# Kernel optimization log

Measured on AMD Instinct MI355X. Metric: run time of the kernel, lower is better.

The kernel has to match this reference:

```python
import jax, jax.numpy as jnp
import numpy as np
import math

B, S, D = 2, 2048, 2048
H = 16
DK = D // H  # 128
DFF = 5440
THETA = 10000.0
EPS = 1e-5


def setup_inputs() -> dict:
    key = jax.random.key(0)
    ks = jax.random.split(key, 9)
    sc = 0.02
    return {
        "x": jax.random.normal(ks[0], (B, S, D), jnp.float32),
        "wq": jax.random.normal(ks[1], (D, D), jnp.float32) * sc,
        "wk": jax.random.normal(ks[2], (D, D), jnp.float32) * sc,
        "wv": jax.random.normal(ks[3], (D, D), jnp.float32) * sc,
        "wo": jax.random.normal(ks[4], (D, D), jnp.float32) * sc,
        "w1": jax.random.normal(ks[5], (DFF, D), jnp.float32) * sc,
        "w2": jax.random.normal(ks[6], (D, DFF), jnp.float32) * sc,
        "w3": jax.random.normal(ks[7], (DFF, D), jnp.float32) * sc,
        "g_attn": jnp.ones((D,), jnp.float32),
        "g_ffn": jnp.ones((D,), jnp.float32),
    }


def _rmsnorm(x, g):
    xf = x.astype(jnp.float32)
    rms = jnp.sqrt(jnp.mean(xf * xf, axis=-1, keepdims=True) + EPS)
    return (xf / rms * g).astype(x.dtype)


def _rope(x):
    # x: (B, H, S, DK)
    pair = jnp.arange(0, DK, 2, dtype=jnp.float32)
    inv_freq = 1.0 / (THETA ** (pair / DK))            # (DK/2,)
    pos = jnp.arange(S, dtype=jnp.float32)
    ang = pos[:, None] * inv_freq[None, :]             # (S, DK/2)
    cos, sin = jnp.cos(ang), jnp.sin(ang)
    xe, xo = x[..., 0::2], x[..., 1::2]
    oe = xe * cos - xo * sin
    oo = xe * sin + xo * cos
    # interleave even/odd back
    out = jnp.stack([oe, oo], axis=-1).reshape(x.shape)
    return out


def reference(x, wq, wk, wv, wo, w1, w2, w3, g_attn, g_ffn):
    # --- attention sublayer ---
    h = _rmsnorm(x, g_attn)
    q = (h @ wq.T).reshape(B, S, H, DK).transpose(0, 2, 1, 3)
    k = (h @ wk.T).reshape(B, S, H, DK).transpose(0, 2, 1, 3)
    v = (h @ wv.T).reshape(B, S, H, DK).transpose(0, 2, 1, 3)
    q = _rope(q)
    k = _rope(k)
    scores = jnp.einsum("bhqd,bhkd->bhqk", q, k) / math.sqrt(DK)
    causal = jnp.tril(jnp.ones((S, S), dtype=bool))
    scores = jnp.where(causal, scores, jnp.finfo(scores.dtype).min)
    attn = jax.nn.softmax(scores, axis=-1)
    o = jnp.einsum("bhqk,bhkd->bhqd", attn, v)
    o = o.transpose(0, 2, 1, 3).reshape(B, S, D)
    x = x + o @ wo.T
    # --- SwiGLU FFN sublayer ---
    h = _rmsnorm(x, g_ffn)
    a = h @ w1.T
    gate = a * jax.nn.sigmoid(a)
    ff = (gate * (h @ w3.T)) @ w2.T
    return x + ff
```

## Files before the change

### kernel.cpp

```cpp
#include <hip/hip_runtime.h>
#include <cstdint>
#include <cstddef>

typedef float  f32x4  __attribute__((ext_vector_type(4)));
typedef __bf16 bf16x8 __attribute__((ext_vector_type(8)));
typedef unsigned short u16x8 __attribute__((ext_vector_type(8)));
typedef unsigned short u16x4 __attribute__((ext_vector_type(4)));

#define DEV static __device__ __forceinline__

DEV unsigned short f2bfu(float f) { __bf16 b = (__bf16)f; return __builtin_bit_cast(unsigned short, b); }
DEV float bfu2f(unsigned short u) { return (float)__builtin_bit_cast(__bf16, u); }
DEV bf16x8 ldb8(const unsigned short* p) { return __builtin_bit_cast(bf16x8, *(const u16x8*)p); }
DEV float fexp(float x) { return __builtin_amdgcn_exp2f(x * 1.44269504f); }

DEV f32x4 mfma16(bf16x8 a, bf16x8 b, f32x4 c) {
  return __builtin_amdgcn_mfma_f32_16x16x32_bf16(a, b, c, 0, 0, 0);
}

DEV void gload16(const void* g, void* l) {
  __builtin_amdgcn_global_load_lds((const unsigned int*)g, (unsigned int*)l, 16, 0, 0);
}

__global__ __launch_bounds__(256) void conv_cat3(
    const float* __restrict__ s0, const float* __restrict__ s1,
    const float* __restrict__ s2, unsigned short* __restrict__ d)
{
  size_t i = (size_t)blockIdx.x * 256 + threadIdx.x;
  size_t e = i * 4;
  const float* s = e < 4194304 ? s0 : (e < 8388608 ? s1 : s2);
  f32x4 v = *(const f32x4*)(s + (e & 4194303));
  u16x4 o = { f2bfu(v.x), f2bfu(v.y), f2bfu(v.z), f2bfu(v.w) };
  *(u16x4*)(d + e) = o;
}

__global__ __launch_bounds__(256) void conv_plain(
    const float* __restrict__ s, unsigned short* __restrict__ d)
{
  size_t e = ((size_t)blockIdx.x * 256 + threadIdx.x) * 4;
  f32x4 v = *(const f32x4*)(s + e);
  u16x4 o = { f2bfu(v.x), f2bfu(v.y), f2bfu(v.z), f2bfu(v.w) };
  *(u16x4*)(d + e) = o;
}

__global__ __launch_bounds__(256) void conv_w13(
    const float* __restrict__ w1, const float* __restrict__ w3,
    unsigned short* __restrict__ d)
{
  size_t i = (size_t)blockIdx.x * 256 + threadIdx.x;
  size_t e = i * 4;
  int n = (int)(e >> 11), kc = (int)(e & 2047);
  int grp = n >> 4;
  const float* s = (grp & 1) ? w3 : w1;
  size_t off = ((size_t)((grp >> 1) * 16 + (n & 15))) * 2048 + kc;
  f32x4 v = *(const f32x4*)(s + off);
  u16x4 o = { f2bfu(v.x), f2bfu(v.y), f2bfu(v.z), f2bfu(v.w) };
  *(u16x4*)(d + e) = o;
}

template<int EPI>
__global__ __launch_bounds__(256) void gemm_f(
    const unsigned short* __restrict__ A, const unsigned short* __restrict__ B,
    void* __restrict__ D0, void* __restrict__ D1, void* __restrict__ D2,
    const float* __restrict__ auxf, const float* __restrict__ cosT,
    const float* __restrict__ sinT, int M, int N, int K)
{
  __shared__ __align__(16) unsigned short As[128 * 64];
  __shared__ __align__(16) unsigned short Bs[128 * 64];
  const int tid = threadIdx.x, lane = tid & 63, w = tid >> 6;
  const int wr = w >> 1, wc = w & 1, l15 = lane & 15, lg = lane >> 4;
  const int m0 = blockIdx.x * 128, n0 = blockIdx.y * 128;

  const int srow  = tid >> 3;
  const int scol8 = (tid & 7) ^ (srow & 7);
  const unsigned short* Asrc = A + (size_t)(m0 + srow) * K + scol8 * 8;
  const unsigned short* Bsrc = B + (size_t)(n0 + srow) * K + scol8 * 8;

  f32x4 zero = {0.f, 0.f, 0.f, 0.f};
  f32x4 acc[4][4];
#pragma unroll
  for (int i = 0; i < 4; i++)
#pragma unroll
    for (int j = 0; j < 4; j++) acc[i][j] = zero;

  for (int k0 = 0; k0 < K; k0 += 64) {
#pragma unroll
    for (int p = 0; p < 4; ++p) {
      gload16(Asrc + (size_t)(p * 32) * K + k0, As + (p * 256 + w * 64) * 8);
      gload16(Bsrc + (size_t)(p * 32) * K + k0, Bs + (p * 256 + w * 64) * 8);
    }
    __syncthreads();
    bf16x8 af[2][4], bfr[2][4];
#pragma unroll
    for (int kk = 0; kk < 2; ++kk) {
#pragma unroll
      for (int i = 0; i < 4; ++i) {
        int rA = wr * 64 + i * 16 + l15;
        af[kk][i]  = ldb8(As + rA * 64 + ((((kk << 2) | lg)) ^ (rA & 7)) * 8);
        int rB = wc * 64 + i * 16 + l15;
        bfr[kk][i] = ldb8(Bs + rB * 64 + ((((kk << 2) | lg)) ^ (rB & 7)) * 8);
      }
    }
#pragma unroll
    for (int kk = 0; kk < 2; ++kk)
#pragma unroll
      for (int mi = 0; mi < 4; mi++)
#pragma unroll
        for (int ni = 0; ni < 4; ni++)
          acc[mi][ni] = mfma16(af[kk][mi], bfr[kk][ni], acc[mi][ni]);
    __syncthreads();
  }

  if constexpr (EPI == 0) {
    unsigned short* qd = (unsigned short*)D0;
    unsigned short* kd = (unsigned short*)D1;
    unsigned short* vd = (unsigned short*)D2;
#pragma unroll
    for (int mi = 0; mi < 4; mi++) {
#pragma unroll
      for (int ni = 0; ni < 4; ni++) {
        int col = n0 + wc * 64 + ni * 16 + l15;
#pragma unroll
        for (int r = 0; r < 4; r++) {
          int row = m0 + wr * 64 + mi * 16 + lg * 4 + r;
          float v = acc[mi][ni][r];
          if (col < 4096) {
            int d = col & 127, pi = d >> 1, sp = row & 2047;
            float c = cosT[sp * 64 + pi], s = sinT[sp * 64 + pi];
            float part = __shfl_xor(v, 1);
            float res = (d & 1) ? (part * s + v * c) : (v * c - part * s);
            unsigned short* dst = (col < 2048) ? qd : kd;
            dst[(size_t)row * 2048 + (col & 2047)] = f2bfu(res);
          } else {
            int vdc = col - 4096;
            vd[((size_t)((row >> 11) * 2048 + vdc)) * 2048 + (row & 2047)] = f2bfu(v);
          }
        }
      }
    }
  } else if constexpr (EPI == 1 || EPI == 3) {
    float* O = (float*)D0;
#pragma unroll
    for (int mi = 0; mi < 4; mi++)
#pragma unroll
      for (int ni = 0; ni < 4; ni++) {
        int col = n0 + wc * 64 + ni * 16 + l15;
#pragma unroll
        for (int r = 0; r < 4; r++) {
          int row = m0 + wr * 64 + mi * 16 + lg * 4 + r;
          size_t ix = (size_t)row * 2048 + col;
          if constexpr (EPI == 1) O[ix] = auxf[ix] + acc[mi][ni][r];
          else                    O[ix] = O[ix] + acc[mi][ni][r];
        }
      }
  } else if constexpr (EPI == 2) {
    unsigned short* G = (unsigned short*)D0;
#pragma unroll
    for (int mi = 0; mi < 4; mi++)
#pragma unroll
      for (int nj = 0; nj < 2; nj++) {
        int outc = (4 * blockIdx.y + 2 * wc + nj) * 16 + l15;
#pragma unroll
        for (int r = 0; r < 4; r++) {
          int row = m0 + wr * 64 + mi * 16 + lg * 4 + r;
          float a = acc[mi][2 * nj][r];
          float c = acc[mi][2 * nj + 1][r];
          float sg = a / (1.0f + fexp(-a));
          G[(size_t)row * 5440 + outc] = f2bfu(sg * c);
        }
      }
  }
}

__global__ __launch_bounds__(256) void rmsnorm_k(
    const float* __restrict__ x, const float* __restrict__ g,
    unsigned short* __restrict__ out)
{
  int row = blockIdx.x, t = threadIdx.x;
  const float* xr = x + (size_t)row * 2048;
  f32x4 v0 = ((const f32x4*)xr)[t];
  f32x4 v1 = ((const f32x4*)xr)[t + 256];
  float ss = v0.x*v0.x + v0.y*v0.y + v0.z*v0.z + v0.w*v0.w
           + v1.x*v1.x + v1.y*v1.y + v1.z*v1.z + v1.w*v1.w;
  __shared__ float red[256];
  red[t] = ss; __syncthreads();
  for (int sh = 128; sh > 0; sh >>= 1) {
    if (t < sh) red[t] += red[t + sh];
    __syncthreads();
  }
  float rinv = rsqrtf(red[0] * (1.0f / 2048.0f) + 1e-5f);
  f32x4 g0 = ((const f32x4*)g)[t];
  f32x4 g1 = ((const f32x4*)g)[t + 256];
  u16x4 o0 = { f2bfu(v0.x*rinv*g0.x), f2bfu(v0.y*rinv*g0.y),
               f2bfu(v0.z*rinv*g0.z), f2bfu(v0.w*rinv*g0.w) };
  u16x4 o1 = { f2bfu(v1.x*rinv*g1.x), f2bfu(v1.y*rinv*g1.y),
               f2bfu(v1.z*rinv*g1.z), f2bfu(v1.w*rinv*g1.w) };
  *(u16x4*)(out + (size_t)row * 2048 + t * 4) = o0;
  *(u16x4*)(out + (size_t)row * 2048 + 1024 + t * 4) = o1;
}

__global__ __launch_bounds__(256) void rope_tab(float* __restrict__ cosT,
                                                float* __restrict__ sinT)
{
  int idx = blockIdx.x * 256 + threadIdx.x;
  int s = idx >> 6, p = idx & 63;
  float ang = (float)s * powf(10000.0f, -(float)p / 64.0f);
  cosT[idx] = cosf(ang);
  sinT[idx] = sinf(ang);
}

__global__ __launch_bounds__(256) void attn_fwd(
    const unsigned short* __restrict__ q, const unsigned short* __restrict__ k,
    const unsigned short* __restrict__ vt, unsigned short* __restrict__ o)
{
  const int S = 2048, Dm = 2048;
  const int tid  = threadIdx.x;
  const int lane = tid & 63;
  const int w    = tid >> 6;
  const int hh   = blockIdx.y, b = blockIdx.z;
  const int l15  = lane & 15, lg = lane >> 4;
  const float SCALE = 0.08838834764831845f;

  __shared__ __align__(16) unsigned short Ks[64 * 128];
  __shared__ __align__(16) unsigned short Vs[128 * 64];
  __shared__ __align__(16) unsigned short Ps[4][16 * 76];

  const unsigned short* kg = k  + ((size_t)(b * S)) * Dm + hh * 128;
  const unsigned short* vg = vt + ((size_t)((b * 16 + hh) * 128)) * S;

  for (int half = 0; half < 2; ++half) {
    const int qt = half ? (31 - blockIdx.x) : blockIdx.x;
    const int r0 = qt * 64;

    bf16x8 qf[4];
    size_t qbase = ((size_t)(b * S + r0 + w * 16 + l15)) * Dm + hh * 128 + lg * 8;
#pragma unroll
    for (int kk = 0; kk < 4; kk++) qf[kk] = ldb8(q + qbase + kk * 32);

    f32x4 zero = {0.f, 0.f, 0.f, 0.f};
    f32x4 accO[8];
#pragma unroll
    for (int dt = 0; dt < 8; dt++) accO[dt] = zero;
    float mrow[4] = {-1e30f, -1e30f, -1e30f, -1e30f};
    float lrow[4] = {0.f, 0.f, 0.f, 0.f};

    int ntile = qt + 1;
    for (int j = 0; j < ntile; ++j) {
      int kv0 = j * 64;
#pragma unroll
      for (int i = 0; i < 4; i++) {
        int idx = i * 256 + tid;
        int row = idx >> 4, slot = idx & 15;
        u16x8 vv = *(const u16x8*)(kg + (size_t)(kv0 + row) * Dm + slot * 8);
        int boff = (row * 256 + slot * 16) ^ ((row & 7) << 4);
        *(u16x8*)((char*)Ks + boff) = vv;
      }
#pragma unroll
      for (int i = 0; i < 4; i++) {
        int idx = i * 256 + tid;
        int row = idx >> 3, slot = idx & 7;
        u16x8 vv = *(const u16x8*)(vg + (size_t)row * S + kv0 + slot * 8);
        int boff = (row * 128 + slot * 16) ^ ((row & 7) << 4);
        *(u16x8*)((char*)Vs + boff) = vv;
      }
      __syncthreads();

      f32x4 sfr[4];
#pragma unroll
      for (int sv = 0; sv < 4; sv++) sfr[sv] = zero;
#pragma unroll
      for (int kk = 0; kk < 4; kk++) {
#pragma unroll
        for (int sv = 0; sv < 4; sv++) {
          int row = sv * 16 + l15;
          int boff = (row * 256 + kk * 64 + lg * 16) ^ ((row & 7) << 4);
          bf16x8 kf = ldb8((const unsigned short*)((const char*)Ks + boff));
          sfr[sv] = mfma16(qf[kk], kf, sfr[sv]);
        }
      }

      float alpha[4];
      float pv[4][4];
#pragma unroll
      for (int r = 0; r < 4; r++) {
        int qr = r0 + w * 16 + lg * 4 + r;
        float a[4];
#pragma unroll
        for (int sv = 0; sv < 4; sv++)
          a[sv] = (kv0 + sv * 16 + l15 <= qr) ? sfr[sv][r] * SCALE : -1e30f;
        float mx = fmaxf(fmaxf(a[0], a[1]), fmaxf(a[2], a[3]));
#pragma unroll
        for (int off = 1; off < 16; off <<= 1) mx = fmaxf(mx, __shfl_xor(mx, off));
        float mnew = fmaxf(mrow[r], mx);
        alpha[r] = fexp(mrow[r] - mnew);
        float ps = 0.f;
#pragma unroll
        for (int sv = 0; sv < 4; sv++) { pv[r][sv] = fexp(a[sv] - mnew); ps += pv[r][sv]; }
#pragma unroll
        for (int off = 1; off < 16; off <<= 1) ps += __shfl_xor(ps, off);
        lrow[r] = lrow[r] * alpha[r] + ps;
        mrow[r] = mnew;
      }
#pragma unroll
      for (int dt = 0; dt < 8; dt++) {
        f32x4 t = accO[dt];
        t[0] *= alpha[0]; t[1] *= alpha[1]; t[2] *= alpha[2]; t[3] *= alpha[3];
        accO[dt] = t;
      }

#pragma unroll
      for (int r = 0; r < 4; r++)
#pragma unroll
        for (int sv = 0; sv < 4; sv++)
          Ps[w][(lg * 4 + r) * 76 + sv * 16 + l15] = f2bfu(pv[r][sv]);

      bf16x8 pa[2];
      pa[0] = ldb8(&Ps[w][l15 * 76 + lg * 8]);
      pa[1] = ldb8(&Ps[w][l15 * 76 + 32 + lg * 8]);
#pragma unroll
      for (int dt = 0; dt < 8; dt++) {
#pragma unroll
        for (int kk = 0; kk < 2; kk++) {
          int row = dt * 16 + l15;
          int boff = (row * 128 + kk * 64 + lg * 16) ^ ((row & 7) << 4);
          bf16x8 vb = ldb8((const unsigned short*)((const char*)Vs + boff));
          accO[dt] = mfma16(pa[kk], vb, accO[dt]);
        }
      }
      __syncthreads();
    }

#pragma unroll
    for (int dt = 0; dt < 8; dt++) {
#pragma unroll
      for (int r = 0; r < 4; r++) {
        int qr = r0 + w * 16 + lg * 4 + r;
        o[((size_t)(b * S + qr)) * Dm + hh * 128 + dt * 16 + l15] =
            f2bfu(accO[dt][r] / lrow[r]);
      }
    }
  }
}

extern "C" void kernel_launch(void* const* d_in, const int* in_sizes, int n_in,
                              void* d_out, int out_size, void* d_ws, size_t ws_size,
                              hipStream_t stream)
{
  const float* x      = (const float*)d_in[0];
  const float* wq     = (const float*)d_in[1];
  const float* wk     = (const float*)d_in[2];
  const float* wv     = (const float*)d_in[3];
  const float* wo     = (const float*)d_in[4];
  const float* w1     = (const float*)d_in[5];
  const float* w2     = (const float*)d_in[6];
  const float* w3     = (const float*)d_in[7];
  const float* g_attn = (const float*)d_in[8];
  const float* g_ffn  = (const float*)d_in[9];
  float* out = (float*)d_out;

  unsigned short* W = (unsigned short*)d_ws;
  unsigned short* h_bf    = W;
  unsigned short* q_bf    = W + 8388608ull;
  unsigned short* k_bf    = W + 16777216ull;
  unsigned short* vt_bf   = W + 25165824ull;
  unsigned short* o_bf    = W + 33554432ull;
  unsigned short* wqkv_bf = W + 41943040ull;
  unsigned short* wo_bf   = W + 54525952ull;
  unsigned short* w13_bf  = W + 58720256ull;
  unsigned short* w2_bf   = W + 81002496ull;
  unsigned short* a1_bf   = q_bf;
  float* cosT = (float*)(W + 92143616ull);
  float* sinT = cosT + 131072;

  dim3 blk(256);
  rope_tab<<<512, blk, 0, stream>>>(cosT, sinT);
  conv_cat3<<<12288, blk, 0, stream>>>(wq, wk, wv, wqkv_bf);
  conv_plain<<<4096, blk, 0, stream>>>(wo, wo_bf);
  conv_w13<<<21760, blk, 0, stream>>>(w1, w3, w13_bf);
  conv_plain<<<10880, blk, 0, stream>>>(w2, w2_bf);

  rmsnorm_k<<<4096, blk, 0, stream>>>(x, g_attn, h_bf);

  gemm_f<0><<<dim3(32, 48), blk, 0, stream>>>(h_bf, wqkv_bf, q_bf, k_bf, vt_bf,
                                              nullptr, cosT, sinT, 4096, 6144, 2048);

  attn_fwd<<<dim3(16, 16, 2), blk, 0, stream>>>(q_bf, k_bf, vt_bf, o_bf);

  gemm_f<1><<<dim3(32, 16), blk, 0, stream>>>(o_bf, wo_bf, out, nullptr, nullptr,
                                              x, nullptr, nullptr, 4096, 2048, 2048);
  rmsnorm_k<<<4096, blk, 0, stream>>>(out, g_ffn, h_bf);

  gemm_f<2><<<dim3(32, 85), blk, 0, stream>>>(h_bf, w13_bf, a1_bf, nullptr, nullptr,
                                              nullptr, nullptr, nullptr, 4096, 10880, 2048);
  gemm_f<3><<<dim3(32, 16), blk, 0, stream>>>(a1_bf, w2_bf, out, nullptr, nullptr,
                                              nullptr, nullptr, nullptr, 4096, 2048, 5440);
}
```

Baseline: 784.5 us.

## Replace GEMM with 256x256-tile, 512-thread, triple-buffered pipelined kernel

Replaces the 128x128 single-buffered GEMM with a 256x256-tile kernel using 8 waves and a three-stage LDS ring fed by global_load_lds. Prefetches two K-steps ahead with explicit vmcnt waits, and splits each K-step into two MFMA halves that alternate with loads under raised wave priority. Remaps block indices so neighbouring tiles share an XCD. The W13 output width is padded to 11008 with an epilogue bounds guard, and the rope tables move into the o_bf buffer. The aim is to hide global-load latency and raise arithmetic intensity per tile, at the cost of one block per CU and fewer blocks for the N=2048 GEMMs (128 tiles).

```diff
diff --git a/kernel.cpp b/kernel.cpp
--- a/kernel.cpp
+++ b/kernel.cpp
@@ -11,7 +11,7 @@
 
 DEV unsigned short f2bfu(float f) { __bf16 b = (__bf16)f; return __builtin_bit_cast(unsigned short, b); }
 DEV float bfu2f(unsigned short u) { return (float)__builtin_bit_cast(__bf16, u); }
-DEV bf16x8 ldb8(const unsigned short* p) { return __builtin_bit_cast(bf16x8, *(const u16x8*)p); }
+DEV bf16x8 ldb8(const void* p) { return __builtin_bit_cast(bf16x8, *(const u16x8*)p); }
 DEV float fexp(float x) { return __builtin_amdgcn_exp2f(x * 1.44269504f); }
 
 DEV f32x4 mfma16(bf16x8 a, bf16x8 b, f32x4 c) {
@@ -21,6 +21,11 @@
 DEV void gload16(const void* g, void* l) {
   __builtin_amdgcn_global_load_lds((const unsigned int*)g, (unsigned int*)l, 16, 0, 0);
 }
+
+#define FENCE() asm volatile("" ::: "memory")
+#define LGKM0() asm volatile("s_waitcnt lgkmcnt(0)" ::: "memory")
+#define VMC4()  asm volatile("s_waitcnt vmcnt(4)" ::: "memory")
+#define VMC0()  asm volatile("s_waitcnt vmcnt(0)" ::: "memory")
 
 __global__ __launch_bounds__(256) void conv_cat3(
     const float* __restrict__ s0, const float* __restrict__ s1,
@@ -59,56 +64,125 @@
 }
 
 template<int EPI>
-__global__ __launch_bounds__(256) void gemm_f(
+__global__ __launch_bounds__(512, 1) void gemm8(
     const unsigned short* __restrict__ A, const unsigned short* __restrict__ B,
     void* __restrict__ D0, void* __restrict__ D1, void* __restrict__ D2,
     const float* __restrict__ auxf, const float* __restrict__ cosT,
     const float* __restrict__ sinT, int M, int N, int K)
 {
-  __shared__ __align__(16) unsigned short As[128 * 64];
-  __shared__ __align__(16) unsigned short Bs[128 * 64];
+  __shared__ __align__(16) char Asb[3 * 16384];
+  __shared__ __align__(16) char Bsb[3 * 16384];
+
   const int tid = threadIdx.x, lane = tid & 63, w = tid >> 6;
-  const int wr = w >> 1, wc = w & 1, l15 = lane & 15, lg = lane >> 4;
-  const int m0 = blockIdx.x * 128, n0 = blockIdx.y * 128;
-
-  const int srow  = tid >> 3;
-  const int scol8 = (tid & 7) ^ (srow & 7);
-  const unsigned short* Asrc = A + (size_t)(m0 + srow) * K + scol8 * 8;
-  const unsigned short* Bsrc = B + (size_t)(n0 + srow) * K + scol8 * 8;
+  const int wm = w >> 2, wn = w & 3;
+  const int l15 = lane & 15, lg = lane >> 4;
+
+  const int nwg = gridDim.x, chunk = nwg >> 3;
+  const int wg = (blockIdx.x & 7) * chunk + (blockIdx.x >> 3);
+  const int MT = M >> 8;
+  const int mt = wg % MT, nt = wg / MT;
+  const int m0 = mt * 256, n0 = nt * 256;
+
+  const int srow0 = tid >> 2, srow1 = 128 + srow0;
+  const int s4d = tid & 3;
+  const int s4s0 = s4d ^ ((srow0 >> 1) & 3);
+  const int s4s1 = s4d ^ ((srow1 >> 1) & 3);
+  const size_t aoff0 = (size_t)(m0 + srow0) * K + s4s0 * 8;
+  const size_t aoff1 = (size_t)(m0 + srow1) * K + s4s1 * 8;
+  const size_t boff0 = (size_t)(n0 + srow0) * K + s4s0 * 8;
+  const size_t boff1 = (size_t)(n0 + srow1) * K + s4s1 * 8;
+  const int d0b = srow0 * 64 + s4d * 16;
+  const int d1b = srow1 * 64 + s4d * 16;
 
   f32x4 zero = {0.f, 0.f, 0.f, 0.f};
-  f32x4 acc[4][4];
-#pragma unroll
-  for (int i = 0; i < 4; i++)
+  f32x4 acc[8][4];
+#pragma unroll
+  for (int i = 0; i < 8; i++)
 #pragma unroll
     for (int j = 0; j < 4; j++) acc[i][j] = zero;
 
-  for (int k0 = 0; k0 < K; k0 += 64) {
-#pragma unroll
-    for (int p = 0; p < 4; ++p) {
-      gload16(Asrc + (size_t)(p * 32) * K + k0, As + (p * 256 + w * 64) * 8);
-      gload16(Bsrc + (size_t)(p * 32) * K + k0, Bs + (p * 256 + w * 64) * 8);
+  const int nkt = K >> 5;
+
+  gload16(A + aoff0, Asb + d0b);
+  gload16(A + aoff1, Asb + d1b);
+  gload16(B + boff0, Bsb + d0b);
+  gload16(B + boff1, Bsb + d1b);
+  gload16(A + aoff0 + 32, Asb + 16384 + d0b);
+  gload16(A + aoff1 + 32, Asb + 16384 + d1b);
+  gload16(B + boff0 + 32, Bsb + 16384 + d0b);
+  gload16(B + boff1 + 32, Bsb + 16384 + d1b);
+  VMC4();
+  FENCE();
+  __builtin_amdgcn_s_barrier();
+
+  int arow[8], aro[8], brow[4], bro[4];
+#pragma unroll
+  for (int mi = 0; mi < 8; mi++) {
+    arow[mi] = wm * 128 + mi * 16 + l15;
+    aro[mi] = arow[mi] * 64 + ((lg ^ ((arow[mi] >> 1) & 3)) << 4);
+  }
+#pragma unroll
+  for (int ni = 0; ni < 4; ni++) {
+    brow[ni] = wn * 64 + ni * 16 + l15;
+    bro[ni] = brow[ni] * 64 + ((lg ^ ((brow[ni] >> 1) & 3)) << 4);
+  }
+
+  int cur = 0, nxt = 2;
+  for (int t = 0; t < nkt; ++t) {
+    const char* As = Asb + cur * 16384;
+    const char* Bs = Bsb + cur * 16384;
+    const bool pf = (t + 2) < nkt;
+    const size_t kpf = (size_t)(t + 2) * 32;
+    char* Apf = Asb + nxt * 16384;
+    char* Bpf = Bsb + nxt * 16384;
+
+    bf16x8 bf_[4], af_[4];
+#pragma unroll
+    for (int ni = 0; ni < 4; ni++) bf_[ni] = ldb8(Bs + bro[ni]);
+#pragma unroll
+    for (int mi = 0; mi < 4; mi++) af_[mi] = ldb8(As + aro[mi]);
+    if (pf) {
+      gload16(A + aoff0 + kpf, Apf + d0b);
+      gload16(A + aoff1 + kpf, Apf + d1b);
     }
-    __syncthreads();
-    bf16x8 af[2][4], bfr[2][4];
-#pragma unroll
-    for (int kk = 0; kk < 2; ++kk) {
-#pragma unroll
-      for (int i = 0; i < 4; ++i) {
-        int rA = wr * 64 + i * 16 + l15;
-        af[kk][i]  = ldb8(As + rA * 64 + ((((kk << 2) | lg)) ^ (rA & 7)) * 8);
-        int rB = wc * 64 + i * 16 + l15;
-        bfr[kk][i] = ldb8(Bs + rB * 64 + ((((kk << 2) | lg)) ^ (rB & 7)) * 8);
-      }
+    FENCE();
+    __builtin_amdgcn_s_barrier();
+    LGKM0();
+    __builtin_amdgcn_sched_barrier(0);
+    __builtin_amdgcn_s_setprio(1);
+#pragma unroll
+    for (int mi = 0; mi < 4; mi++)
+#pragma unroll
+      for (int ni = 0; ni < 4; ni++)
+        acc[mi][ni] = mfma16(af_[mi], bf_[ni], acc[mi][ni]);
+    __builtin_amdgcn_s_setprio(0);
+    FENCE();
+    __builtin_amdgcn_s_barrier();
+
+    bf16x8 ag_[4];
+#pragma unroll
+    for (int mi = 0; mi < 4; mi++) ag_[mi] = ldb8(As + aro[mi + 4]);
+    if (pf) {
+      gload16(B + boff0 + kpf, Bpf + d0b);
+      gload16(B + boff1 + kpf, Bpf + d1b);
     }
-#pragma unroll
-    for (int kk = 0; kk < 2; ++kk)
-#pragma unroll
-      for (int mi = 0; mi < 4; mi++)
-#pragma unroll
-        for (int ni = 0; ni < 4; ni++)
-          acc[mi][ni] = mfma16(af[kk][mi], bfr[kk][ni], acc[mi][ni]);
-    __syncthreads();
+    FENCE();
+    __builtin_amdgcn_s_barrier();
+    LGKM0();
+    __builtin_amdgcn_sched_barrier(0);
+    __builtin_amdgcn_s_setprio(1);
+#pragma unroll
+    for (int mi = 0; mi < 4; mi++)
+#pragma unroll
+      for (int ni = 0; ni < 4; ni++)
+        acc[mi + 4][ni] = mfma16(ag_[mi], bf_[ni], acc[mi + 4][ni]);
+    __builtin_amdgcn_s_setprio(0);
+    if (pf) { VMC4(); } else { VMC0(); }
+    FENCE();
+    __builtin_amdgcn_s_barrier();
+
+    cur = cur == 2 ? 0 : cur + 1;
+    nxt = nxt == 2 ? 0 : nxt + 1;
   }
 
   if constexpr (EPI == 0) {
@@ -116,13 +190,13 @@
     unsigned short* kd = (unsigned short*)D1;
     unsigned short* vd = (unsigned short*)D2;
 #pragma unroll
-    for (int mi = 0; mi < 4; mi++) {
+    for (int mi = 0; mi < 8; mi++) {
 #pragma unroll
       for (int ni = 0; ni < 4; ni++) {
-        int col = n0 + wc * 64 + ni * 16 + l15;
+        int col = n0 + wn * 64 + ni * 16 + l15;
 #pragma unroll
         for (int r = 0; r < 4; r++) {
-          int row = m0 + wr * 64 + mi * 16 + lg * 4 + r;
+          int row = m0 + wm * 128 + mi * 16 + lg * 4 + r;
           float v = acc[mi][ni][r];
           if (col < 4096) {
             int d = col & 127, pi = d >> 1, sp = row & 2047;
@@ -141,13 +215,13 @@
   } else if constexpr (EPI == 1 || EPI == 3) {
     float* O = (float*)D0;
 #pragma unroll
-    for (int mi = 0; mi < 4; mi++)
+    for (int mi = 0; mi < 8; mi++)
 #pragma unroll
       for (int ni = 0; ni < 4; ni++) {
-        int col = n0 + wc * 64 + ni * 16 + l15;
+        int col = n0 + wn * 64 + ni * 16 + l15;
 #pragma unroll
         for (int r = 0; r < 4; r++) {
-          int row = m0 + wr * 64 + mi * 16 + lg * 4 + r;
+          int row = m0 + wm * 128 + mi * 16 + lg * 4 + r;
           size_t ix = (size_t)row * 2048 + col;
           if constexpr (EPI == 1) O[ix] = auxf[ix] + acc[mi][ni][r];
           else                    O[ix] = O[ix] + acc[mi][ni][r];
@@ -156,13 +230,14 @@
   } else if constexpr (EPI == 2) {
     unsigned short* G = (unsigned short*)D0;
 #pragma unroll
-    for (int mi = 0; mi < 4; mi++)
+    for (int mi = 0; mi < 8; mi++)
 #pragma unroll
       for (int nj = 0; nj < 2; nj++) {
-        int outc = (4 * blockIdx.y + 2 * wc + nj) * 16 + l15;
+        int outc = (nt * 8 + wn * 2 + nj) * 16 + l15;
+        if (outc >= 5440) continue;
 #pragma unroll
         for (int r = 0; r < 4; r++) {
-          int row = m0 + wr * 64 + mi * 16 + lg * 4 + r;
+          int row = m0 + wm * 128 + mi * 16 + lg * 4 + r;
           float a = acc[mi][2 * nj][r];
           float c = acc[mi][2 * nj + 1][r];
           float sg = a / (1.0f + fexp(-a));
@@ -367,9 +442,9 @@
   unsigned short* wqkv_bf = W + 41943040ull;
   unsigned short* wo_bf   = W + 54525952ull;
   unsigned short* w13_bf  = W + 58720256ull;
-  unsigned short* w2_bf   = W + 81002496ull;
+  unsigned short* w2_bf   = W + 81264640ull;
   unsigned short* a1_bf   = q_bf;
-  float* cosT = (float*)(W + 92143616ull);
+  float* cosT = (float*)o_bf;
   float* sinT = cosT + 131072;
 
   dim3 blk(256);
@@ -381,17 +456,17 @@
 
   rmsnorm_k<<<4096, blk, 0, stream>>>(x, g_attn, h_bf);
 
-  gemm_f<0><<<dim3(32, 48), blk, 0, stream>>>(h_bf, wqkv_bf, q_bf, k_bf, vt_bf,
-                                              nullptr, cosT, sinT, 4096, 6144, 2048);
+  gemm8<0><<<dim3(384), dim3(512), 0, stream>>>(h_bf, wqkv_bf, q_bf, k_bf, vt_bf,
+                                                nullptr, cosT, sinT, 4096, 6144, 2048);
 
   attn_fwd<<<dim3(16, 16, 2), blk, 0, stream>>>(q_bf, k_bf, vt_bf, o_bf);
 
-  gemm_f<1><<<dim3(32, 16), blk, 0, stream>>>(o_bf, wo_bf, out, nullptr, nullptr,
-                                              x, nullptr, nullptr, 4096, 2048, 2048);
+  gemm8<1><<<dim3(128), dim3(512), 0, stream>>>(o_bf, wo_bf, out, nullptr, nullptr,
+                                                x, nullptr, nullptr, 4096, 2048, 2048);
   rmsnorm_k<<<4096, blk, 0, stream>>>(out, g_ffn, h_bf);
 
-  gemm_f<2><<<dim3(32, 85), blk, 0, stream>>>(h_bf, w13_bf, a1_bf, nullptr, nullptr,
-                                              nullptr, nullptr, nullptr, 4096, 10880, 2048);
-  gemm_f<3><<<dim3(32, 16), blk, 0, stream>>>(a1_bf, w2_bf, out, nullptr, nullptr,
-                                              nullptr, nullptr, nullptr, 4096, 2048, 5440);
-}
+  gemm8<2><<<dim3(688), dim3(512), 0, stream>>>(h_bf, w13_bf, a1_bf, nullptr, nullptr,
+                                                nullptr, nullptr, nullptr, 4096, 11008, 2048);
+  gemm8<3><<<dim3(128), dim3(512), 0, stream>>>(a1_bf, w2_bf, out, nullptr, nullptr,
+                                                nullptr, nullptr, nullptr, 4096, 2048, 5440);
+}
```

After: 853.7 us. 1.09x slower.
